# Performance work log

Measured on AMD Instinct MI355X. Metric: run time of the kernel, lower is better.

The kernel has to match this reference:

```python
import jax, jax.numpy as jnp
import numpy as np

B, H, N = 128, 512, 1024

def setup_inputs() -> dict:
    key = jax.random.key(0)
    ks = jax.random.split(key, 9)
    s = 1.0 / np.sqrt(H)
    return {
        "mc_hidden": jax.random.normal(ks[0], (B, H), jnp.float32),
        "sn_hidden": jax.random.normal(ks[1], (B, H, N), jnp.float32),
        "attn_W": jax.random.normal(ks[2], (H, 2 * H), jnp.float32) * s,
        "attn_v": jax.random.normal(ks[3], (H,), jnp.float32) * s,
        "ptr_v": jax.random.normal(ks[4], (H,), jnp.float32) * s,
        "fc1_W": jax.random.normal(ks[5], (H, 2 * H), jnp.float32) * s,
        "fc1_b": jax.random.normal(ks[6], (H,), jnp.float32) * s,
        "fc2_W": jax.random.normal(ks[7], (H, H), jnp.float32) * s,
        "fc2_b": jax.random.normal(ks[8], (H,), jnp.float32) * s,
    }


def reference(mc_hidden, sn_hidden, attn_W, attn_v, ptr_v, fc1_W, fc1_b, fc2_W, fc2_b):
    # ---- Attention (Bahdanau-style additive scoring) ----
    # hidden: (B, 2H, N) = cat(sn_hidden, mc expanded along N) on dim 1
    mc_exp = jnp.broadcast_to(mc_hidden[:, :, None], sn_hidden.shape)  # (B,H,N)
    hidden = jnp.concatenate((sn_hidden, mc_exp), axis=1)              # (B,2H,N)
    # W @ hidden -> (B,H,N); v @ tanh(.) -> (B,N)
    scores = jnp.einsum('h,bhn->bn', attn_v,
                        jnp.tanh(jnp.einsum('hk,bkn->bhn', attn_W, hidden)))
    attns = jax.nn.softmax(scores, axis=-1)                            # (B,N)
    # ---- Context + pointer scoring ----
    context = jnp.einsum('bn,bhn->bh', attns, sn_hidden)               # (B,H)
    x = jnp.concatenate((mc_hidden, context), axis=1)                  # (B,2H)
    out = jax.nn.relu(x @ fc1_W.T + fc1_b)                             # (B,H)
    out = jax.nn.relu(out @ fc2_W.T + fc2_b)                           # (B,H)
    probs = jnp.einsum('h,bhn->bn', ptr_v,
                       jnp.tanh(sn_hidden + out[:, :, None]))          # (B,N)
    return probs
```

## Files before the change

### kernel.cpp

```cpp
#include <hip/hip_runtime.h>
#include <hip/hip_bf16.h>

#define Bn 128
#define Hd 512
#define Nn 1024

typedef __attribute__((ext_vector_type(8))) short short8;
typedef __attribute__((ext_vector_type(4))) float f32x4;

#define GLOAD_LDS16(gptr, lptr)                                                     \
    __builtin_amdgcn_global_load_lds(                                               \
        (const __attribute__((address_space(1))) void*)(gptr),                      \
        (__attribute__((address_space(3))) void*)(lptr), 16, 0, 0)

__device__ __forceinline__ float bf2f(unsigned u) {
    unsigned v = u << 16;
    float f;
    __builtin_memcpy(&f, &v, 4);
    return f;
}

__device__ __forceinline__ unsigned short f2bf(float f) {
    unsigned x;
    __builtin_memcpy(&x, &f, 4);
    unsigned r = x + 0x7fffu + ((x >> 16) & 1u);
    return (unsigned short)(r >> 16);
}

__device__ __forceinline__ float wave_sum(float v) {
    v += __shfl_xor(v, 32);
    v += __shfl_xor(v, 16);
    v += __shfl_xor(v, 8);
    v += __shfl_xor(v, 4);
    v += __shfl_xor(v, 2);
    v += __shfl_xor(v, 1);
    return v;
}

__device__ __forceinline__ float tanh_fast(float x) {
    float e = __expf(2.0f * x);
    return 1.0f - 2.0f * __builtin_amdgcn_rcpf(e + 1.0f);
}

__global__ void convert_W_kernel(const float* __restrict__ attn_W,
                                 unsigned short* __restrict__ Wb) {
    int idx = (blockIdx.x * 256 + threadIdx.x) * 8;
    int h = idx >> 9;
    int k = idx & 511;
    const float* p = attn_W + (size_t)h * 1024 + k;
    float4 v0 = *(const float4*)p;
    float4 v1 = *(const float4*)(p + 4);
    unsigned short t[8] = {f2bf(v0.x), f2bf(v0.y), f2bf(v0.z), f2bf(v0.w),
                           f2bf(v1.x), f2bf(v1.y), f2bf(v1.z), f2bf(v1.w)};
    *(uint4*)(Wb + idx) = *(uint4*)t;
}

__global__ void transpose_sn_kernel(const float* __restrict__ sn,
                                    unsigned short* __restrict__ snT) {
    __shared__ unsigned ldsb[32 * 132];
    int bid = blockIdx.x;
    int b = bid >> 6;
    int kt = (bid >> 3) & 7;
    int nt = bid & 7;
    int k0 = kt << 6, n0 = nt << 7;
    int t = threadIdx.x;

    int kp_l = t >> 5;
    int n4 = (t & 31) * 4;
#pragma unroll
    for (int j = 0; j < 4; ++j) {
        int kp = j * 8 + kp_l;
        const float* p0 = sn + ((size_t)(b * Hd + k0 + 2 * kp)) * Nn + n0 + n4;
        float4 f0 = *(const float4*)p0;
        float4 f1 = *(const float4*)(p0 + Nn);
        unsigned u[4];
        u[0] = (unsigned)f2bf(f0.x) | ((unsigned)f2bf(f1.x) << 16);
        u[1] = (unsigned)f2bf(f0.y) | ((unsigned)f2bf(f1.y) << 16);
        u[2] = (unsigned)f2bf(f0.z) | ((unsigned)f2bf(f1.z) << 16);
        u[3] = (unsigned)f2bf(f0.w) | ((unsigned)f2bf(f1.w) << 16);
        *(uint4*)&ldsb[kp * 132 + n4] = *(uint4*)u;
    }
    __syncthreads();

    int c = t & 7;
#pragma unroll
    for (int it = 0; it < 4; ++it) {
        int n = (t >> 3) + it * 32;
        unsigned u[4];
#pragma unroll
        for (int i = 0; i < 4; ++i) u[i] = ldsb[(c * 4 + i) * 132 + n];
        unsigned short* dst = snT + ((size_t)(b * Nn) + n0 + n) * Hd + k0 + c * 8;
        *(uint4*)dst = *(uint4*)u;
    }
}

__global__ void mc_term_kernel(const float* __restrict__ mc,
                               const float* __restrict__ attn_W,
                               float* __restrict__ mc_term) {
    int wg = (blockIdx.x * blockDim.x + threadIdx.x) >> 6;
    int lane = threadIdx.x & 63;
    int b = wg >> 9;
    int h = wg & 511;
    const float* m = mc + b * Hd + lane * 8;
    const float* w = attn_W + (size_t)h * 1024 + 512 + lane * 8;
    float4 m0 = *(const float4*)m, m1 = *(const float4*)(m + 4);
    float4 w0 = *(const float4*)w, w1 = *(const float4*)(w + 4);
    float acc = m0.x * w0.x + m0.y * w0.y + m0.z * w0.z + m0.w * w0.w +
                m1.x * w1.x + m1.y * w1.y + m1.z * w1.z + m1.w * w1.w;
    acc = wave_sum(acc);
    if (lane == 0) mc_term[b * Hd + h] = acc;
}

__global__ __launch_bounds__(256, 2)
void attn_score_kernel(const unsigned short* __restrict__ snT,
                       const unsigned short* __restrict__ Wb,
                       const float* __restrict__ attn_v,
                       const float* __restrict__ mc_term,
                       float* __restrict__ scores) {
    __shared__ __align__(16) unsigned short A_lds[512 * 64];
    __shared__ __align__(16) unsigned short B_lds[64 * 64];
    __shared__ float av_s[512];
    __shared__ float mct_s[512];
    __shared__ float ssum[64];

    const int b = blockIdx.x >> 4;
    const int n0 = (blockIdx.x & 15) << 6;
    const int tid = threadIdx.x;
    const int lane = tid & 63;
    const int wid = tid >> 6;
    const int quad = lane >> 4;
    const int l15 = lane & 15;
    const int m0 = wid * 128;

    av_s[tid] = attn_v[tid];
    av_s[tid + 256] = attn_v[tid + 256];
    mct_s[tid] = mc_term[b * Hd + tid];
    mct_s[tid + 256] = mc_term[b * Hd + tid + 256];
    if (tid < 64) ssum[tid] = 0.f;

    f32x4 acc[8][4];
#pragma unroll
    for (int i = 0; i < 8; ++i)
#pragma unroll
        for (int j = 0; j < 4; ++j) {
            f32x4 z = {0.f, 0.f, 0.f, 0.f};
            acc[i][j] = z;
        }

    const int r8 = lane >> 3;
    const int csw = ((lane & 7) ^ r8) * 16;
    const char* Wg = (const char*)Wb;
    const char* Bg = (const char*)snT + ((size_t)(b * Nn + n0)) * 1024;
    const int key = l15 & 7;

    for (int k0 = 0; k0 < 512; k0 += 64) {
#pragma unroll
        for (int i = 0; i < 16; ++i) {
            const int row = m0 + i * 8;
            GLOAD_LDS16(Wg + (size_t)(row + r8) * 1024 + k0 * 2 + csw,
                        (char*)A_lds + row * 128);
        }
#pragma unroll
        for (int i = 0; i < 2; ++i) {
            const int row = wid * 16 + i * 8;
            GLOAD_LDS16(Bg + (size_t)(row + r8) * 1024 + k0 * 2 + csw,
                        (char*)B_lds + row * 128);
        }
        __syncthreads();
#pragma unroll
        for (int kk = 0; kk < 2; ++kk) {
            const int cb = quad + kk * 4;
            short8 bfr[4], afr[8];
#pragma unroll
            for (int nt = 0; nt < 4; ++nt) {
                const int n = nt * 16 + l15;
                bfr[nt] = *(const short8*)((const char*)B_lds + n * 128 + ((cb ^ key) * 16));
            }
#pragma unroll
            for (int mt = 0; mt < 8; ++mt) {
                const int m = m0 + mt * 16 + l15;
                afr[mt] = *(const short8*)((const char*)A_lds + m * 128 + ((cb ^ key) * 16));
            }
#pragma unroll
            for (int mt = 0; mt < 8; ++mt)
#pragma unroll
                for (int nt = 0; nt < 4; ++nt)
                    acc[mt][nt] = __builtin_amdgcn_mfma_f32_16x16x32_bf16(afr[mt], bfr[nt], acc[mt][nt], 0, 0, 0);
        }
        __syncthreads();
    }

    float s[4] = {0.f, 0.f, 0.f, 0.f};
#pragma unroll
    for (int mt = 0; mt < 8; ++mt) {
        int hb = m0 + mt * 16 + quad * 4;
#pragma unroll
        for (int r = 0; r < 4; ++r) {
            float av = av_s[hb + r];
            float mcv = mct_s[hb + r];
#pragma unroll
            for (int nt = 0; nt < 4; ++nt)
                s[nt] += av * tanh_fast(acc[mt][nt][r] + mcv);
        }
    }
#pragma unroll
    for (int nt = 0; nt < 4; ++nt) {
        float v = s[nt];
        v += __shfl_xor(v, 16);
        v += __shfl_xor(v, 32);
        if (lane < 16) atomicAdd(&ssum[nt * 16 + l15], v);
    }
    __syncthreads();
    if (tid < 64) scores[b * Nn + n0 + tid] = ssum[tid];
}

__global__ void softmax_kernel(float* __restrict__ scores) {
    const int b = blockIdx.x;
    const int tid = threadIdx.x;
    const int lane = tid & 63, wid = tid >> 6;
    __shared__ float red[4];
    float v[4];
#pragma unroll
    for (int i = 0; i < 4; ++i) v[i] = scores[b * Nn + tid + i * 256];
    float m = fmaxf(fmaxf(v[0], v[1]), fmaxf(v[2], v[3]));
#pragma unroll
    for (int off = 32; off >= 1; off >>= 1) m = fmaxf(m, __shfl_xor(m, off));
    if (lane == 0) red[wid] = m;
    __syncthreads();
    m = fmaxf(fmaxf(red[0], red[1]), fmaxf(red[2], red[3]));
    __syncthreads();
    float s = 0.f;
#pragma unroll
    for (int i = 0; i < 4; ++i) {
        v[i] = __expf(v[i] - m);
        s += v[i];
    }
    s = wave_sum(s);
    if (lane == 0) red[wid] = s;
    __syncthreads();
    s = red[0] + red[1] + red[2] + red[3];
    float inv = __builtin_amdgcn_rcpf(s);
#pragma unroll
    for (int i = 0; i < 4; ++i) scores[b * Nn + tid + i * 256] = v[i] * inv;
}

__global__ void context_kernel(const unsigned short* __restrict__ snT,
                               const float* __restrict__ attns,
                               float* __restrict__ context) {
    int b = blockIdx.x >> 3;
    int nc = (blockIdx.x & 7) << 7;
    int t = threadIdx.x;
    __shared__ float a_s[128];
    if (t < 128) a_s[t] = attns[b * Nn + nc + t];
    __syncthreads();
    const unsigned short* base = snT + ((size_t)(b * Nn) + nc) * Hd + t * 2;
    float acc0 = 0.f, acc1 = 0.f;
#pragma unroll 4
    for (int i = 0; i < 128; ++i) {
        unsigned d = *(const unsigned*)(base + (size_t)i * Hd);
        float a = a_s[i];
        acc0 += a * bf2f(d & 0xffffu);
        acc1 += a * bf2f(d >> 16);
    }
    atomicAdd(&context[b * Hd + 2 * t], acc0);
    atomicAdd(&context[b * Hd + 2 * t + 1], acc1);
}

__global__ void fc1_kernel(const float* __restrict__ mc,
                           const float* __restrict__ ctx,
                           const float* __restrict__ fc1_W,
                           const float* __restrict__ fc1_b,
                           float* __restrict__ out1) {
    int wg = (blockIdx.x * blockDim.x + threadIdx.x) >> 6;
    int lane = threadIdx.x & 63;
    int b = wg >> 9, h = wg & 511;
    const float* wr = fc1_W + (size_t)h * 1024;
    float acc = 0.f;
    {
        float4 w0 = *(const float4*)(wr + lane * 8);
        float4 w1 = *(const float4*)(wr + lane * 8 + 4);
        float4 x0 = *(const float4*)(mc + b * Hd + lane * 8);
        float4 x1 = *(const float4*)(mc + b * Hd + lane * 8 + 4);
        acc += w0.x * x0.x + w0.y * x0.y + w0.z * x0.z + w0.w * x0.w;
        acc += w1.x * x1.x + w1.y * x1.y + w1.z * x1.z + w1.w * x1.w;
    }
    {
        float4 w0 = *(const float4*)(wr + 512 + lane * 8);
        float4 w1 = *(const float4*)(wr + 512 + lane * 8 + 4);
        float4 x0 = *(const float4*)(ctx + b * Hd + lane * 8);
        float4 x1 = *(const float4*)(ctx + b * Hd + lane * 8 + 4);
        acc += w0.x * x0.x + w0.y * x0.y + w0.z * x0.z + w0.w * x0.w;
        acc += w1.x * x1.x + w1.y * x1.y + w1.z * x1.z + w1.w * x1.w;
    }
    acc = wave_sum(acc);
    if (lane == 0) out1[b * Hd + h] = fmaxf(acc + fc1_b[h], 0.f);
}

__global__ void fc2_kernel(const float* __restrict__ out1,
                           const float* __restrict__ fc2_W,
                           const float* __restrict__ fc2_b,
                           float* __restrict__ out2) {
    int wg = (blockIdx.x * blockDim.x + threadIdx.x) >> 6;
    int lane = threadIdx.x & 63;
    int b = wg >> 9, h = wg & 511;
    const float* wr = fc2_W + (size_t)h * 512 + lane * 8;
    float4 w0 = *(const float4*)wr;
    float4 w1 = *(const float4*)(wr + 4);
    float4 x0 = *(const float4*)(out1 + b * Hd + lane * 8);
    float4 x1 = *(const float4*)(out1 + b * Hd + lane * 8 + 4);
    float acc = w0.x * x0.x + w0.y * x0.y + w0.z * x0.z + w0.w * x0.w +
                w1.x * x1.x + w1.y * x1.y + w1.z * x1.z + w1.w * x1.w;
    acc = wave_sum(acc);
    if (lane == 0) out2[b * Hd + h] = fmaxf(acc + fc2_b[h], 0.f);
}

__global__ void final_kernel(const unsigned short* __restrict__ snT,
                             const float* __restrict__ ptr_v,
                             const float* __restrict__ out2,
                             float* __restrict__ probs) {
    int b = blockIdx.x >> 4;
    int n0 = (blockIdx.x & 15) << 6;
    int t = threadIdx.x;
    int n = n0 + (t >> 2), p = t & 3;
    __shared__ float pv_s[512], o2_s[512];
    pv_s[t] = ptr_v[t];
    pv_s[t + 256] = ptr_v[t + 256];
    o2_s[t] = out2[b * Hd + t];
    o2_s[t + 256] = out2[b * Hd + t + 256];
    __syncthreads();
    const unsigned short* row = snT + ((size_t)(b * Nn) + n) * Hd + p * 8;
    float a = 0.f;
#pragma unroll 4
    for (int j = 0; j < 16; ++j) {
        uint4 d = *(const uint4*)(row + j * 32);
        int hb = p * 8 + j * 32;
        const unsigned* u = (const unsigned*)&d;
#pragma unroll
        for (int q = 0; q < 4; ++q) {
            int h = hb + q * 2;
            float x0 = bf2f(u[q] & 0xffffu);
            float x1 = bf2f(u[q] >> 16);
            a += pv_s[h] * tanh_fast(x0 + o2_s[h]);
            a += pv_s[h + 1] * tanh_fast(x1 + o2_s[h + 1]);
        }
    }
    a += __shfl_xor(a, 1);
    a += __shfl_xor(a, 2);
    if (p == 0) probs[b * Nn + n] = a;
}

extern "C" void kernel_launch(void* const* d_in, const int* in_sizes, int n_in,
                              void* d_out, int out_size, void* d_ws, size_t ws_size,
                              hipStream_t stream) {
    const float* mc  = (const float*)d_in[0];
    const float* sn  = (const float*)d_in[1];
    const float* aW  = (const float*)d_in[2];
    const float* av  = (const float*)d_in[3];
    const float* pv  = (const float*)d_in[4];
    const float* f1W = (const float*)d_in[5];
    const float* f1b = (const float*)d_in[6];
    const float* f2W = (const float*)d_in[7];
    const float* f2b = (const float*)d_in[8];

    unsigned short* snT = (unsigned short*)d_ws;
    unsigned short* Wb  = snT + (size_t)Bn * Nn * Hd;
    float* fws     = (float*)(Wb + 512 * 512);
    float* mc_term = fws;
    float* scores  = mc_term + Bn * Hd;
    float* context = scores + Bn * Nn;
    float* out1    = context + Bn * Hd;
    float* out2    = out1 + Bn * Hd;
    float* probs   = (float*)d_out;

    hipMemsetAsync(context, 0, Bn * Hd * sizeof(float), stream);
    convert_W_kernel<<<dim3(128), dim3(256), 0, stream>>>(aW, Wb);
    transpose_sn_kernel<<<dim3(8192), dim3(256), 0, stream>>>(sn, snT);
    mc_term_kernel<<<dim3(16384), dim3(256), 0, stream>>>(mc, aW, mc_term);
    attn_score_kernel<<<dim3(2048), dim3(256), 0, stream>>>(snT, Wb, av, mc_term, scores);
    softmax_kernel<<<dim3(128), dim3(256), 0, stream>>>(scores);
    context_kernel<<<dim3(1024), dim3(256), 0, stream>>>(snT, scores, context);
    fc1_kernel<<<dim3(16384), dim3(256), 0, stream>>>(mc, context, f1W, f1b, out1);
    fc2_kernel<<<dim3(16384), dim3(256), 0, stream>>>(out1, f2W, f2b, out2);
    final_kernel<<<dim3(2048), dim3(256), 0, stream>>>(snT, pv, out2, probs);
}
```

Measured before the change: 565.8 us.

## Double-buffer W tiles in LDS and stream sn fragments directly to registers

The attention-score GEMM moves to 512-thread blocks covering 128 columns, with each wave owning a 128x64 output sub-tile. W tiles are double-buffered in LDS with a K-step of 32, so the next tile's load overlaps the current MFMAs and one barrier per step is dropped. The sn operand is now read straight from global memory into registers, prefetched two steps ahead, which removes the B tile from LDS. The costs are higher register pressure, a different LDS swizzle, and uncoalesced per-lane global reads for B.

```diff
diff --git a/kernel.cpp b/kernel.cpp
--- a/kernel.cpp
+++ b/kernel.cpp
@@ -111,32 +111,33 @@
     if (lane == 0) mc_term[b * Hd + h] = acc;
 }
 
-__global__ __launch_bounds__(256, 2)
+__global__ __launch_bounds__(512, 2)
 void attn_score_kernel(const unsigned short* __restrict__ snT,
                        const unsigned short* __restrict__ Wb,
                        const float* __restrict__ attn_v,
                        const float* __restrict__ mc_term,
                        float* __restrict__ scores) {
-    __shared__ __align__(16) unsigned short A_lds[512 * 64];
-    __shared__ __align__(16) unsigned short B_lds[64 * 64];
+    __shared__ __align__(16) unsigned short A_lds[2][512 * 32];
     __shared__ float av_s[512];
     __shared__ float mct_s[512];
-    __shared__ float ssum[64];
-
-    const int b = blockIdx.x >> 4;
-    const int n0 = (blockIdx.x & 15) << 6;
+    __shared__ float ssum[128];
+
+    const int b = blockIdx.x >> 3;
+    const int ntile = blockIdx.x & 7;
+    const int n0 = ntile << 7;
     const int tid = threadIdx.x;
     const int lane = tid & 63;
-    const int wid = tid >> 6;
+    const int w = tid >> 6;
     const int quad = lane >> 4;
     const int l15 = lane & 15;
-    const int m0 = wid * 128;
-
-    av_s[tid] = attn_v[tid];
-    av_s[tid + 256] = attn_v[tid + 256];
-    mct_s[tid] = mc_term[b * Hd + tid];
-    mct_s[tid + 256] = mc_term[b * Hd + tid + 256];
-    if (tid < 64) ssum[tid] = 0.f;
+    const int m0w = (w >> 1) * 128;
+    const int nb = (w & 1) * 64;
+
+    if (tid < 512) {
+        av_s[tid] = attn_v[tid];
+        mct_s[tid] = mc_term[b * Hd + tid];
+    }
+    if (tid < 128) ssum[tid] = 0.f;
 
     f32x4 acc[8][4];
 #pragma unroll
@@ -147,53 +148,59 @@
             acc[i][j] = z;
         }
 
-    const int r8 = lane >> 3;
-    const int csw = ((lane & 7) ^ r8) * 16;
-    const char* Wg = (const char*)Wb;
-    const char* Bg = (const char*)snT + ((size_t)(b * Nn + n0)) * 1024;
-    const int key = l15 & 7;
-
-    for (int k0 = 0; k0 < 512; k0 += 64) {
-#pragma unroll
-        for (int i = 0; i < 16; ++i) {
-            const int row = m0 + i * 8;
-            GLOAD_LDS16(Wg + (size_t)(row + r8) * 1024 + k0 * 2 + csw,
-                        (char*)A_lds + row * 128);
-        }
-#pragma unroll
-        for (int i = 0; i < 2; ++i) {
-            const int row = wid * 16 + i * 8;
-            GLOAD_LDS16(Bg + (size_t)(row + r8) * 1024 + k0 * 2 + csw,
-                        (char*)B_lds + row * 128);
-        }
+    const int r_l = lane >> 2;
+    const int c_l = lane & 3;
+    const int csw = ((c_l ^ (r_l & 3)) << 4);
+    const char* Ag = (const char*)Wb;
+    const short* Bg = (const short*)snT + ((size_t)(b * Nn + n0)) * Hd;
+    const int ard = ((quad ^ (l15 & 3)) << 4) + l15 * 64 + m0w * 64;
+
+#pragma unroll
+    for (int i = 0; i < 4; ++i) {
+        const int R = w * 64 + i * 16;
+        GLOAD_LDS16(Ag + (size_t)(R + r_l) * 1024 + csw,
+                    (char*)A_lds[0] + R * 64);
+    }
+    short8 bfr[2][4];
+#pragma unroll
+    for (int nt = 0; nt < 4; ++nt) {
+        const short* p = Bg + (size_t)(nb + nt * 16 + l15) * Hd + quad * 8;
+        bfr[0][nt] = *(const short8*)(p);
+        bfr[1][nt] = *(const short8*)(p + 32);
+    }
+
+#pragma unroll
+    for (int it = 0; it < 16; ++it) {
+        const int p = it & 1;
         __syncthreads();
-#pragma unroll
-        for (int kk = 0; kk < 2; ++kk) {
-            const int cb = quad + kk * 4;
-            short8 bfr[4], afr[8];
-#pragma unroll
-            for (int nt = 0; nt < 4; ++nt) {
-                const int n = nt * 16 + l15;
-                bfr[nt] = *(const short8*)((const char*)B_lds + n * 128 + ((cb ^ key) * 16));
+        if (it < 15) {
+#pragma unroll
+            for (int i = 0; i < 4; ++i) {
+                const int R = w * 64 + i * 16;
+                GLOAD_LDS16(Ag + (size_t)(R + r_l) * 1024 + (it + 1) * 64 + csw,
+                            (char*)A_lds[p ^ 1] + R * 64);
             }
-#pragma unroll
-            for (int mt = 0; mt < 8; ++mt) {
-                const int m = m0 + mt * 16 + l15;
-                afr[mt] = *(const short8*)((const char*)A_lds + m * 128 + ((cb ^ key) * 16));
-            }
-#pragma unroll
-            for (int mt = 0; mt < 8; ++mt)
-#pragma unroll
-                for (int nt = 0; nt < 4; ++nt)
-                    acc[mt][nt] = __builtin_amdgcn_mfma_f32_16x16x32_bf16(afr[mt], bfr[nt], acc[mt][nt], 0, 0, 0);
-        }
-        __syncthreads();
+        }
+        short8 afr[8];
+#pragma unroll
+        for (int mt = 0; mt < 8; ++mt)
+            afr[mt] = *(const short8*)((const char*)A_lds[p] + mt * 1024 + ard);
+#pragma unroll
+        for (int mt = 0; mt < 8; ++mt)
+#pragma unroll
+            for (int nt = 0; nt < 4; ++nt)
+                acc[mt][nt] = __builtin_amdgcn_mfma_f32_16x16x32_bf16(afr[mt], bfr[p][nt], acc[mt][nt], 0, 0, 0);
+        if (it < 14) {
+#pragma unroll
+            for (int nt = 0; nt < 4; ++nt)
+                bfr[p][nt] = *(const short8*)(Bg + (size_t)(nb + nt * 16 + l15) * Hd + (it + 2) * 32 + quad * 8);
+        }
     }
 
     float s[4] = {0.f, 0.f, 0.f, 0.f};
 #pragma unroll
     for (int mt = 0; mt < 8; ++mt) {
-        int hb = m0 + mt * 16 + quad * 4;
+        int hb = m0w + mt * 16 + quad * 4;
 #pragma unroll
         for (int r = 0; r < 4; ++r) {
             float av = av_s[hb + r];
@@ -208,10 +215,10 @@
         float v = s[nt];
         v += __shfl_xor(v, 16);
         v += __shfl_xor(v, 32);
-        if (lane < 16) atomicAdd(&ssum[nt * 16 + l15], v);
-    }
-    __syncthreads();
-    if (tid < 64) scores[b * Nn + n0 + tid] = ssum[tid];
+        if (lane < 16) atomicAdd(&ssum[nb + nt * 16 + l15], v);
+    }
+    __syncthreads();
+    if (tid < 128) scores[b * Nn + n0 + tid] = ssum[tid];
 }
 
 __global__ void softmax_kernel(float* __restrict__ scores) {
@@ -376,7 +383,7 @@
     convert_W_kernel<<<dim3(128), dim3(256), 0, stream>>>(aW, Wb);
     transpose_sn_kernel<<<dim3(8192), dim3(256), 0, stream>>>(sn, snT);
     mc_term_kernel<<<dim3(16384), dim3(256), 0, stream>>>(mc, aW, mc_term);
-    attn_score_kernel<<<dim3(2048), dim3(256), 0, stream>>>(snT, Wb, av, mc_term, scores);
+    attn_score_kernel<<<dim3(1024), dim3(512), 0, stream>>>(snT, Wb, av, mc_term, scores);
     softmax_kernel<<<dim3(128), dim3(256), 0, stream>>>(scores);
     context_kernel<<<dim3(1024), dim3(256), 0, stream>>>(snT, scores, context);
     fc1_kernel<<<dim3(16384), dim3(256), 0, stream>>>(mc, context, f1W, f1b, out1);
```

Result: slower. 609.6 us (+7.8%).
